# Optimization experiments

Measured on AMD Instinct MI355X. Metric: run time of the kernel, lower is better.

Reference implementation:

```python
import jax, jax.numpy as jnp
import numpy as np

VOXEL_DIM = (128, 128, 64)   # nx, ny, nz
VOXEL_SIZE = 0.04            # meters per voxel


def setup_inputs() -> dict:
    key = jax.random.key(0)
    k1, = jax.random.split(key, 1)
    b, c, h, w = 2, 32, 120, 160
    features = jax.random.normal(k1, (b, c, h, w), dtype=jnp.float32)

    # Realistic projection = intrinsics @ extrinsics (already divided by backbone stride)
    K = np.array([[145.0, 0.0, 80.0],
                  [0.0, 145.0, 60.0],
                  [0.0, 0.0, 1.0]], dtype=np.float32)
    proj = np.zeros((b, 3, 4), dtype=np.float32)
    for i in range(b):
        Rt = np.eye(3, 4, dtype=np.float32)
        Rt[:, 3] = [0.0, 0.0, 0.5 + 0.1 * i]  # camera slightly behind the volume
        proj[i] = K @ Rt

    origin = jnp.tile(jnp.array([[-2.56, -2.56, 0.0]], dtype=jnp.float32), (b, 1))
    return {"projection": jnp.asarray(proj), "features": features, "origin": origin}


def reference(projection, features, origin):
    b, c, h, w = features.shape
    nx, ny, nz = VOXEL_DIM
    n = nx * ny * nz

    # voxel grid coordinates, flattened in (x, y, z) 'ij' order -> (3, N)
    gx, gy, gz = jnp.meshgrid(jnp.arange(nx), jnp.arange(ny), jnp.arange(nz), indexing="ij")
    coords = jnp.stack([gx.ravel(), gy.ravel(), gz.ravel()], axis=0).astype(jnp.float32)

    # world = coords * voxel_size + origin ; homogeneous (b, 4, N)
    world = coords[None] * VOXEL_SIZE + origin[:, :, None]
    world = jnp.concatenate([world, jnp.ones_like(world[:, :1])], axis=1)

    # camera coords: (b, 3, N)
    camera = jnp.einsum("bij,bjn->bin", projection, world)
    px = jnp.round(camera[:, 0] / camera[:, 2]).astype(jnp.int32)
    py = jnp.round(camera[:, 1] / camera[:, 2]).astype(jnp.int32)
    pz = camera[:, 2]

    valid = (px >= 0) & (py >= 0) & (px < w) & (py < h) & (pz > 0)  # (b, N)

    # gather image features at (py, px), masked to zero where invalid
    idx = jnp.clip(py, 0, h - 1) * w + jnp.clip(px, 0, w - 1)       # (b, N)
    feat_flat = features.reshape(b, c, h * w)
    gathered = jnp.take_along_axis(feat_flat, idx[:, None, :], axis=2)  # (b, c, N)
    volume = jnp.where(valid[:, None, :], gathered, jnp.zeros((), features.dtype))

    volume = volume.reshape(b, c, nx, ny, nz)
    valid = valid.reshape(b, 1, nx, ny, nz)
    return volume, valid
```

## Files before the change

kernel.cpp:

```cpp
#include <hip/hip_runtime.h>
#include <math.h>

#define NX 128
#define NY 128
#define NZ 64
#define NVOX (NX * NY * NZ)
#define NC 32
#define FH 120
#define FW 160
#define FHW (FH * FW)
#define VOXSZ 0.04f
#define NB 2
#define T_BYTES ((size_t)NB * FHW * NC * 4)

__global__ __launch_bounds__(256) void transpose_feat_kernel(
    const float* __restrict__ feat, float* __restrict__ T)
{
    const int t = blockIdx.x * 256 + threadIdx.x;
    const int b = t / FHW;
    const int pix = t - b * FHW;
    const float* fb = feat + (size_t)b * NC * FHW + pix;
    float v[NC];
    #pragma unroll
    for (int c = 0; c < NC; ++c) v[c] = fb[(size_t)c * FHW];
    float4* row = (float4*)(T + ((size_t)b * FHW + pix) * NC);
    #pragma unroll
    for (int r = 0; r < NC / 4; ++r)
        row[r] = make_float4(v[4*r], v[4*r+1], v[4*r+2], v[4*r+3]);
}

__global__ __launch_bounds__(256) void voxel_backproject_kernel(
    const float* __restrict__ proj,
    const float* __restrict__ T,
    const float* __restrict__ origin,
    float* __restrict__ out)
{
#pragma clang fp contract(off)
    const int tid = blockIdx.x * 256 + threadIdx.x;
    const int b = tid >> 20;
    const int n = tid & (NVOX - 1);
    const int i = n >> 13;
    const int j = (n >> 6) & (NY - 1);
    const int k = n & (NZ - 1);

    const float* P = proj + b * 12;
    const float ox = origin[b * 3 + 0];
    const float oy = origin[b * 3 + 1];
    const float oz = origin[b * 3 + 2];

    const float wx = (float)i * VOXSZ + ox;
    const float wy = (float)j * VOXSZ + oy;
    const float wz = (float)k * VOXSZ + oz;

    const float tx = P[0] * wx + P[1] * wy;
    const float ty = P[4] * wx + P[5] * wy;
    const float tz = P[8] * wx + P[9] * wy;

    const float cx = tx + (P[2]  * wz + P[3]);
    const float cy = ty + (P[6]  * wz + P[7]);
    const float cz = tz + (P[10] * wz + P[11]);

    const float qx = cx / cz;
    const float qy = cy / cz;
    const int px = __float2int_rn(qx);
    const int py = __float2int_rn(qy);
    const bool v = (px >= 0) & (py >= 0) & (px < FW) & (py < FH) & (cz > 0.0f);

    float4 r0 = {0,0,0,0}, r1 = {0,0,0,0}, r2 = {0,0,0,0}, r3 = {0,0,0,0};
    float4 r4 = {0,0,0,0}, r5 = {0,0,0,0}, r6 = {0,0,0,0}, r7 = {0,0,0,0};
    if (v) {
        const int idx = py * FW + px;
        const float4* row = (const float4*)(T + ((size_t)b * FHW + idx) * NC);
        r0 = row[0]; r1 = row[1]; r2 = row[2]; r3 = row[3];
        r4 = row[4]; r5 = row[5]; r6 = row[6]; r7 = row[7];
    }

    float* ob = out + (size_t)b * NC * NVOX + n;
    const float4 rr[8] = {r0,r1,r2,r3,r4,r5,r6,r7};
    #pragma unroll
    for (int t = 0; t < 8; ++t) {
        ob[(size_t)(4*t + 0) * NVOX] = rr[t].x;
        ob[(size_t)(4*t + 1) * NVOX] = rr[t].y;
        ob[(size_t)(4*t + 2) * NVOX] = rr[t].z;
        ob[(size_t)(4*t + 3) * NVOX] = rr[t].w;
    }
    out[(size_t)NB * NC * NVOX + (size_t)b * NVOX + n] = v ? 1.0f : 0.0f;
}

extern "C" void kernel_launch(void* const* d_in, const int* in_sizes, int n_in,
                              void* d_out, int out_size, void* d_ws, size_t ws_size,
                              hipStream_t stream) {
    const float* proj   = (const float*)d_in[0];
    const float* feat   = (const float*)d_in[1];
    const float* origin = (const float*)d_in[2];
    float* out = (float*)d_out;

    float* T = (float*)d_ws;
    transpose_feat_kernel<<<(NB * FHW) / 256, 256, 0, stream>>>(feat, T);
    const int total = NB * NVOX;
    voxel_backproject_kernel<<<total / 256, 256, 0, stream>>>(proj, T, origin, out);
}
```

Baseline: 53.73 us.

## Split backprojection into index projection pass and channel-major float4 gather pass

Replaces the feature transpose plus per-voxel 32-channel gather with two kernels. The first computes each voxel's projected pixel index and valid mask and stores the index in workspace. The second has each thread handle four consecutive voxels of one channel, gathering from the original channel-major features and writing float4 stores. This targets the scattered 32-stride per-channel stores, at the cost of an extra index buffer round trip and more gather instructions. The old path is kept as a fallback when the workspace is too small.

```diff
diff --git a/kernel.cpp b/kernel.cpp
--- a/kernel.cpp
+++ b/kernel.cpp
@@ -11,7 +11,72 @@
 #define FHW (FH * FW)
 #define VOXSZ 0.04f
 #define NB 2
+#define IDX_BYTES ((size_t)NB * NVOX * 4)
 #define T_BYTES ((size_t)NB * FHW * NC * 4)
+
+__global__ __launch_bounds__(256) void project_kernel(
+    const float* __restrict__ proj,
+    const float* __restrict__ origin,
+    int* __restrict__ idxbuf,
+    float* __restrict__ out)
+{
+#pragma clang fp contract(off)
+    const int tid = blockIdx.x * 256 + threadIdx.x;
+    const int b = tid >> 20;
+    const int n = tid & (NVOX - 1);
+    const int i = n >> 13;
+    const int j = (n >> 6) & (NY - 1);
+    const int k = n & (NZ - 1);
+
+    const float* P = proj + b * 12;
+    const float ox = origin[b * 3 + 0];
+    const float oy = origin[b * 3 + 1];
+    const float oz = origin[b * 3 + 2];
+
+    const float wx = (float)i * VOXSZ + ox;
+    const float wy = (float)j * VOXSZ + oy;
+    const float wz = (float)k * VOXSZ + oz;
+
+    const float tx = P[0] * wx + P[1] * wy;
+    const float ty = P[4] * wx + P[5] * wy;
+    const float tz = P[8] * wx + P[9] * wy;
+
+    const float cx = tx + (P[2]  * wz + P[3]);
+    const float cy = ty + (P[6]  * wz + P[7]);
+    const float cz = tz + (P[10] * wz + P[11]);
+
+    const float qx = cx / cz;
+    const float qy = cy / cz;
+    const int px = __float2int_rn(qx);
+    const int py = __float2int_rn(qy);
+    const bool v = (px >= 0) & (py >= 0) & (px < FW) & (py < FH) & (cz > 0.0f);
+
+    idxbuf[tid] = v ? (py * FW + px) : -1;
+    out[(size_t)NB * NC * NVOX + (size_t)b * NVOX + n] = v ? 1.0f : 0.0f;
+}
+
+__global__ __launch_bounds__(256) void scatter_kernel(
+    const float* __restrict__ feat,
+    const int* __restrict__ idxbuf,
+    float* __restrict__ out)
+{
+    const int tid = blockIdx.x * 256 + threadIdx.x;
+    const int n4 = tid & ((NVOX >> 2) - 1);
+    const int c  = (tid >> 18) & (NC - 1);
+    const int b  = tid >> 23;
+    const int n0 = n4 * 4;
+
+    const int4 id4 = *(const int4*)(idxbuf + (size_t)b * NVOX + n0);
+    const float* fp = feat + ((size_t)b * NC + c) * FHW;
+
+    float4 r;
+    r.x = (id4.x >= 0) ? fp[id4.x] : 0.0f;
+    r.y = (id4.y >= 0) ? fp[id4.y] : 0.0f;
+    r.z = (id4.z >= 0) ? fp[id4.z] : 0.0f;
+    r.w = (id4.w >= 0) ? fp[id4.w] : 0.0f;
+
+    *(float4*)(out + ((size_t)b * NC + c) * NVOX + n0) = r;
+}
 
 __global__ __launch_bounds__(256) void transpose_feat_kernel(
     const float* __restrict__ feat, float* __restrict__ T)
@@ -47,19 +112,15 @@
     const float ox = origin[b * 3 + 0];
     const float oy = origin[b * 3 + 1];
     const float oz = origin[b * 3 + 2];
-
     const float wx = (float)i * VOXSZ + ox;
     const float wy = (float)j * VOXSZ + oy;
     const float wz = (float)k * VOXSZ + oz;
-
     const float tx = P[0] * wx + P[1] * wy;
     const float ty = P[4] * wx + P[5] * wy;
     const float tz = P[8] * wx + P[9] * wy;
-
     const float cx = tx + (P[2]  * wz + P[3]);
     const float cy = ty + (P[6]  * wz + P[7]);
     const float cz = tz + (P[10] * wz + P[11]);
-
     const float qx = cx / cz;
     const float qy = cy / cz;
     const int px = __float2int_rn(qx);
@@ -74,7 +135,6 @@
         r0 = row[0]; r1 = row[1]; r2 = row[2]; r3 = row[3];
         r4 = row[4]; r5 = row[5]; r6 = row[6]; r7 = row[7];
     }
-
     float* ob = out + (size_t)b * NC * NVOX + n;
     const float4 rr[8] = {r0,r1,r2,r3,r4,r5,r6,r7};
     #pragma unroll
@@ -95,8 +155,13 @@
     const float* origin = (const float*)d_in[2];
     float* out = (float*)d_out;
 
-    float* T = (float*)d_ws;
-    transpose_feat_kernel<<<(NB * FHW) / 256, 256, 0, stream>>>(feat, T);
-    const int total = NB * NVOX;
-    voxel_backproject_kernel<<<total / 256, 256, 0, stream>>>(proj, T, origin, out);
+    if (ws_size >= IDX_BYTES) {
+        int* idxbuf = (int*)d_ws;
+        project_kernel<<<(NB * NVOX) / 256, 256, 0, stream>>>(proj, origin, idxbuf, out);
+        scatter_kernel<<<(NB * NC * (NVOX / 4)) / 256, 256, 0, stream>>>(feat, idxbuf, out);
+    } else {
+        float* T = (float*)d_ws;
+        transpose_feat_kernel<<<(NB * FHW) / 256, 256, 0, stream>>>(feat, T);
+        voxel_backproject_kernel<<<(NB * NVOX) / 256, 256, 0, stream>>>(proj, T, origin, out);
+    }
 }
```

New measurement: 92.08 us. 1.71x slower.
